# Kernel optimization log

Hardware: AMD Instinct MI355X
Metric: run time of the kernel (lower is better)

Reference implementation:

```python
import jax, jax.numpy as jnp
import numpy as np

N_NODES = 50000
N_EDGES = 500000
F_NODE, F_EDGE, D, H, L = 7, 8, 64, 128, 3


def setup_inputs() -> dict:
    key = jax.random.key(0)
    ks = jax.random.split(key, 24)
    g = lambda k, shp, fan: jax.random.normal(k, shp, dtype=jnp.float32) * (1.0 / np.sqrt(fan))
    inp = {
        "node_features": jax.random.normal(ks[0], (N_NODES, F_NODE), dtype=jnp.float32),
        "edge_attr": jax.random.normal(ks[1], (N_EDGES, F_EDGE), dtype=jnp.float32),
        "embed_W": g(ks[2], (F_NODE, D), F_NODE),
        "embed_b": jnp.zeros((D,), jnp.float32),
        "msg_W1": g(ks[3], (L, 2 * D + F_EDGE, H), 2 * D + F_EDGE),
        "msg_b1": jnp.zeros((L, H), jnp.float32),
        "msg_W2": g(ks[4], (L, H, H), H),
        "msg_b2": jnp.zeros((L, H), jnp.float32),
        "upd_W": g(ks[5], (L, D + H, D), D + H),
        "upd_b": jnp.zeros((L, D), jnp.float32),
        "ln_g": jnp.ones((L, D), jnp.float32),
        "ln_b": jnp.zeros((L, D), jnp.float32),
        "pred_W1": g(ks[6], (2 * D + F_EDGE, H), 2 * D + F_EDGE),
        "pred_b1": jnp.zeros((H,), jnp.float32),
        "pred_W2": g(ks[7], (H, H // 2), H),
        "pred_b2": jnp.zeros((H // 2,), jnp.float32),
        "pred_W3": g(ks[8], (H // 2, 1), H // 2),
        "pred_b3": jnp.zeros((1,), jnp.float32),
        "edge_index": jax.random.randint(ks[9], (2, N_EDGES), 0, N_NODES, dtype=jnp.int32),
    }
    return inp


def _layer_norm(x, g, b, eps=1e-5):
    mu = jnp.mean(x, axis=-1, keepdims=True)
    var = jnp.mean((x - mu) ** 2, axis=-1, keepdims=True)
    return (x - mu) * jax.lax.rsqrt(var + eps) * g + b


def reference(node_features, edge_attr, embed_W, embed_b, msg_W1, msg_b1, msg_W2, msg_b2,
              upd_W, upd_b, ln_g, ln_b, pred_W1, pred_b1, pred_W2, pred_b2, pred_W3, pred_b3,
              edge_index):
    src, dst = edge_index[0], edge_index[1]
    n_nodes = node_features.shape[0]
    # node embedding (dropout = identity in eval)
    x = jax.nn.relu(node_features @ embed_W + embed_b)
    ones_e = jnp.ones((edge_attr.shape[0],), dtype=x.dtype)
    counts = jax.ops.segment_sum(ones_e, dst, num_segments=n_nodes)[:, None]  # [N,1]
    for l in range(L):
        # gather + concat -> message MLP over edges
        edge_in = jnp.concatenate([x[src], x[dst], edge_attr], axis=1)  # [E, 2D+Fe]
        h = jax.nn.relu(edge_in @ msg_W1[l] + msg_b1[l])
        messages = h @ msg_W2[l] + msg_b2[l]  # [E, H]
        # scatter-add aggregation + mean normalize
        agg = jax.ops.segment_sum(messages, dst, num_segments=n_nodes)
        agg = agg / (counts + 1e-6)
        # update MLP with residual
        upd_in = jnp.concatenate([x, agg], axis=1)  # [N, D+H]
        x = x + jax.nn.relu(upd_in @ upd_W[l] + upd_b[l])
        x = _layer_norm(x, ln_g[l], ln_b[l])
    # edge predictor
    edge_in = jnp.concatenate([x[src], x[dst], edge_attr], axis=1)
    h = jax.nn.relu(edge_in @ pred_W1 + pred_b1)
    h = jax.nn.relu(h @ pred_W2 + pred_b2)
    pred = jnp.tanh(h @ pred_W3 + pred_b3)[:, 0]  # [E]
    return pred
```

## Files before the change

kernel.cpp:

```cpp
#include <hip/hip_runtime.h>

#define NN 50000
#define NE 500000
#define NBLK ((NN + 1023) / 1024)

typedef __attribute__((ext_vector_type(8))) short bf8_t;
typedef __attribute__((ext_vector_type(4))) float f4_t;
#define MFMA16(a, b, c) __builtin_amdgcn_mfma_f32_16x16x32_bf16(a, b, c, 0, 0, 0)

__device__ __forceinline__ short f2bf(float f) {
  unsigned u = __float_as_uint(f);
  u += 0x7fffu + ((u >> 16) & 1u);
  return (short)(u >> 16);
}
__device__ __forceinline__ float bf_lo(unsigned u) { return __uint_as_float(u << 16); }
__device__ __forceinline__ float bf_hi(unsigned u) { return __uint_as_float(u & 0xffff0000u); }
__device__ __forceinline__ float bf2f(short s) {
  return __uint_as_float(((unsigned)(unsigned short)s) << 16);
}

__global__ __launch_bounds__(256) void k_zero_i(int* __restrict__ p, int n)
{
  for (int i = blockIdx.x * 256 + threadIdx.x; i < n; i += gridDim.x * 256)
    p[i] = 0;
}

__global__ __launch_bounds__(256) void k_prep_w1(const float* __restrict__ W1,
                                                 short* __restrict__ w1f)
{
  int idx = blockIdx.x * 256 + threadIdx.x;
  if (idx >= 3 * 5 * 8 * 64 * 8) return;
  int l = idx / 20480;
  int rem = idx - l * 20480;
  int ks = rem / 4096;
  int nt = (rem >> 9) & 7;
  int lane = (rem >> 3) & 63;
  int j = rem & 7;
  int k = ks * 32 + (lane >> 4) * 8 + j;
  int n = nt * 16 + (lane & 15);
  float v = (k < 136) ? W1[(size_t)l * 136 * 128 + (size_t)k * 128 + n] : 0.f;
  w1f[idx] = f2bf(v);
}
__global__ __launch_bounds__(256) void k_prep_w2(const float* __restrict__ W2,
                                                 short* __restrict__ w2f)
{
  int idx = blockIdx.x * 256 + threadIdx.x;
  if (idx >= 3 * 4 * 8 * 64 * 8) return;
  int l = idx / 16384;
  int rem = idx - l * 16384;
  int ks = rem / 4096;
  int nt = (rem >> 9) & 7;
  int lane = (rem >> 3) & 63;
  int j = rem & 7;
  int k = ks * 32 + (lane >> 4) * 8 + j;
  int n = nt * 16 + (lane & 15);
  w2f[idx] = f2bf(W2[(size_t)l * 128 * 128 + (size_t)k * 128 + n]);
}
__global__ __launch_bounds__(256) void k_prep_wu(const float* __restrict__ Wu,
                                                 short* __restrict__ wuf)
{
  int idx = blockIdx.x * 256 + threadIdx.x;
  if (idx >= 3 * 6 * 4 * 64 * 8) return;
  int l = idx / 12288;
  int rem = idx - l * 12288;
  int ks = rem / 2048;
  int nt = (rem >> 9) & 3;
  int lane = (rem >> 3) & 63;
  int j = rem & 7;
  int k = ks * 32 + (lane >> 4) * 8 + j;
  int n = nt * 16 + (lane & 15);
  wuf[idx] = f2bf(Wu[(size_t)l * 192 * 64 + (size_t)k * 64 + n]);
}
__global__ __launch_bounds__(256) void k_prep_pw1(const float* __restrict__ W1,
                                                  short* __restrict__ wf)
{
  int idx = blockIdx.x * 256 + threadIdx.x;
  if (idx >= 5 * 8 * 64 * 8) return;
  int ks = idx / 4096;
  int nt = (idx >> 9) & 7;
  int lane = (idx >> 3) & 63;
  int j = idx & 7;
  int k = ks * 32 + (lane >> 4) * 8 + j;
  int n = nt * 16 + (lane & 15);
  float v = (k < 136) ? W1[(size_t)k * 128 + n] : 0.f;
  wf[idx] = f2bf(v);
}
__global__ __launch_bounds__(256) void k_prep_pw2(const float* __restrict__ W2,
                                                  short* __restrict__ wf)
{
  int idx = blockIdx.x * 256 + threadIdx.x;
  if (idx >= 4 * 4 * 64 * 8) return;
  int ks = idx / 2048;
  int nt = (idx >> 9) & 3;
  int lane = (idx >> 3) & 63;
  int j = idx & 7;
  int k = ks * 32 + (lane >> 4) * 8 + j;
  int n = nt * 16 + (lane & 15);
  wf[idx] = f2bf(W2[(size_t)k * 64 + n]);
}
__global__ __launch_bounds__(256) void k_prep_ea(const float* __restrict__ ea,
                                                 short* __restrict__ eab)
{
  int i = blockIdx.x * 256 + threadIdx.x;
  if (i >= NE * 2) return;
  float4 v = *(const float4*)&ea[(size_t)i * 4];
  short4 o;
  o.x = f2bf(v.x); o.y = f2bf(v.y); o.z = f2bf(v.z); o.w = f2bf(v.w);
  *(short4*)&eab[(size_t)i * 4] = o;
}

__global__ __launch_bounds__(256) void k_embed(
    const float* __restrict__ nf, const float* __restrict__ We,
    const float* __restrict__ be, float* __restrict__ x, short* __restrict__ xb)
{
  int idx = blockIdx.x * 256 + threadIdx.x;
  int n = idx >> 4, g = idx & 15;
  if (n >= NN) return;
  int j0 = g * 4;
  float4 b4 = *(const float4*)&be[j0];
  float a0 = b4.x, a1 = b4.y, a2 = b4.z, a3 = b4.w;
  #pragma unroll
  for (int k = 0; k < 7; ++k) {
    float v = nf[n * 7 + k];
    float4 w = *(const float4*)&We[k * 64 + j0];
    a0 += v * w.x; a1 += v * w.y; a2 += v * w.z; a3 += v * w.w;
  }
  a0 = fmaxf(a0, 0.f); a1 = fmaxf(a1, 0.f); a2 = fmaxf(a2, 0.f); a3 = fmaxf(a3, 0.f);
  *(float4*)&x[(size_t)n * 64 + j0] = make_float4(a0, a1, a2, a3);
  short4 o; o.x = f2bf(a0); o.y = f2bf(a1); o.z = f2bf(a2); o.w = f2bf(a3);
  *(short4*)&xb[(size_t)n * 64 + j0] = o;
}

__global__ __launch_bounds__(256) void k_hist(const int* __restrict__ dst, int* __restrict__ cnt)
{
  int e = blockIdx.x * 256 + threadIdx.x;
  if (e < NE) atomicAdd(&cnt[dst[e]], 1);
}

__global__ __launch_bounds__(1024) void k_scan1(const int* __restrict__ cnt,
                                                int* __restrict__ loc, int* __restrict__ bsum)
{
  __shared__ int ws[16];
  const int b = blockIdx.x, t = threadIdx.x;
  const int i = b * 1024 + t;
  const int ln = t & 63, wv = t >> 6;
  int v = (i < NN) ? cnt[i] : 0;
  int s = v;
  #pragma unroll
  for (int off = 1; off < 64; off <<= 1) {
    int u = __shfl_up(s, off, 64);
    if (ln >= off) s += u;
  }
  if (ln == 63) ws[wv] = s;
  __syncthreads();
  if (wv == 0) {
    int wsum = (ln < 16) ? ws[ln] : 0;
    #pragma unroll
    for (int off = 1; off < 16; off <<= 1) {
      int u = __shfl_up(wsum, off, 64);
      if (ln >= off) wsum += u;
    }
    if (ln < 16) ws[ln] = wsum;
  }
  __syncthreads();
  int woff = (wv > 0) ? ws[wv - 1] : 0;
  int incl = s + woff;
  if (i < NN) loc[i] = incl - v;
  if (t == 1023) bsum[b] = incl;
}
__global__ __launch_bounds__(64) void k_scan2(const int* __restrict__ bsum,
                                              int* __restrict__ boff)
{
  const int ln = threadIdx.x;
  int v = (ln < NBLK) ? bsum[ln] : 0;
  int s = v;
  #pragma unroll
  for (int off = 1; off < 64; off <<= 1) {
    int u = __shfl_up(s, off, 64);
    if (ln >= off) s += u;
  }
  if (ln < NBLK) boff[ln] = s - v;
}
__global__ __launch_bounds__(256) void k_scan3(const int* __restrict__ loc,
                                               const int* __restrict__ boff,
                                               int* __restrict__ ptr,
                                               int* __restrict__ cur)
{
  int i = blockIdx.x * 256 + threadIdx.x;
  if (i < NN) {
    int v = loc[i] + boff[i >> 10];
    ptr[i] = v;
    cur[i] = v;
  }
}

__global__ __launch_bounds__(256) void k_fill(
    const int* __restrict__ src, const int* __restrict__ dst,
    const short* __restrict__ eab, int* __restrict__ cur,
    int* __restrict__ srcc, short* __restrict__ eac)
{
  int e = blockIdx.x * 256 + threadIdx.x;
  if (e < 128) srcc[NE + e] = 0;
  if (e < NE) {
    int d = dst[e];
    int s = atomicAdd(&cur[d], 1);
    srcc[s] = src[e];
    *(bf8_t*)(eac + (size_t)s * 8) = *(const bf8_t*)(eab + (size_t)e * 8);
  }
}

__global__ __launch_bounds__(256, 4) void k_y1(
    const short* __restrict__ xb, const short* __restrict__ w1f_l,
    const float* __restrict__ b1,
    short* __restrict__ y1s, short* __restrict__ y1d)
{
  const int t = threadIdx.x;
  const int wv = t >> 6, l = t & 63;
  const int m16 = l & 15, g = l >> 4;
  const int nb = blockIdx.x * 64 + wv * 16;
  if (nb >= NN) return;
  int row = nb + m16; if (row >= NN) row = NN - 1;
  const short* xr = xb + (size_t)row * 64;
  bf8_t a0 = *(const bf8_t*)(xr + g * 8);
  bf8_t a1 = *(const bf8_t*)(xr + 32 + g * 8);
  const short* wl = w1f_l + l * 8;

  f4_t accS[8], accD[8];
  #pragma unroll
  for (int nt = 0; nt < 8; ++nt) {
    float bv = b1[nt * 16 + m16];
    accS[nt] = (f4_t){0.f, 0.f, 0.f, 0.f};
    accD[nt] = (f4_t){bv, bv, bv, bv};
  }
  #pragma unroll
  for (int nt = 0; nt < 8; ++nt) {
    bf8_t b0 = *(const bf8_t*)(wl + (0 * 8 + nt) * 512);
    bf8_t b1f = *(const bf8_t*)(wl + (1 * 8 + nt) * 512);
    bf8_t b2f = *(const bf8_t*)(wl + (2 * 8 + nt) * 512);
    bf8_t b3f = *(const bf8_t*)(wl + (3 * 8 + nt) * 512);
    accS[nt] = MFMA16(a0, b0, accS[nt]);
    accS[nt] = MFMA16(a1, b1f, accS[nt]);
    accD[nt] = MFMA16(a0, b2f, accD[nt]);
    accD[nt] = MFMA16(a1, b3f, accD[nt]);
  }
  #pragma unroll
  for (int nt = 0; nt < 8; ++nt) {
    #pragma unroll
    for (int r = 0; r < 4; ++r) {
      int n = nb + g * 4 + r;
      if (n < NN) {
        y1s[(size_t)n * 128 + nt * 16 + m16] = f2bf(accS[nt][r]);
        y1d[(size_t)n * 128 + nt * 16 + m16] = f2bf(accD[nt][r]);
      }
    }
  }
}

__global__ __launch_bounds__(256, 4) void k_msg_n(
    const short* __restrict__ y1s, const short* __restrict__ y1d,
    const short* __restrict__ eac, const int* __restrict__ srcc,
    const int* __restrict__ ptr, const int* __restrict__ cnt,
    const float* __restrict__ W1l,
    float* __restrict__ hagg)
{
  const int t = threadIdx.x;
  const int wv = t >> 6, ln = t & 63;
  const int n = blockIdx.x * 4 + wv;
  if (n >= NN) return;

  float we[8][2];
  #pragma unroll
  for (int f = 0; f < 8; ++f) {
    we[f][0] = W1l[(128 + f) * 128 + 2 * ln];
    we[f][1] = W1l[(128 + f) * 128 + 2 * ln + 1];
  }
  const int p0 = ptr[n];
  const int p1 = p0 + cnt[n];

  unsigned ydu = *(const unsigned*)(y1d + (size_t)n * 128 + 2 * ln);
  const float yd0 = bf_lo(ydu), yd1 = bf_hi(ydu);

  float s0 = 0.f, s1 = 0.f;
  for (int e = p0; e < p1; ++e) {
    int s = srcc[e];
    unsigned ysu = *(const unsigned*)(y1s + (size_t)s * 128 + 2 * ln);
    bf8_t eav = *(const bf8_t*)(eac + (size_t)e * 8);
    float z0 = 0.f, z1 = 0.f;
    #pragma unroll
    for (int f = 0; f < 8; ++f) {
      float ef = bf2f(eav[f]);
      z0 += ef * we[f][0];
      z1 += ef * we[f][1];
    }
    s0 += fmaxf(bf_lo(ysu) + yd0 + z0, 0.f);
    s1 += fmaxf(bf_hi(ysu) + yd1 + z1, 0.f);
  }
  *(float2*)(hagg + (size_t)n * 128 + 2 * ln) = make_float2(s0, s1);
}

__global__ __launch_bounds__(256, 4) void k_node(
    float* __restrict__ x, short* __restrict__ xb,
    const float* __restrict__ hagg, const int* __restrict__ cnt,
    const short* __restrict__ w2f_l, const float* __restrict__ b2,
    const short* __restrict__ wuf_l, const float* __restrict__ bu,
    const float* __restrict__ lng, const float* __restrict__ lnb)
{
  __shared__ short sH[4 * 16 * 136];
  const int t = threadIdx.x;
  const int wv = t >> 6, l = t & 63;
  const int m16 = l & 15, g = l >> 4;
  const int nb = blockIdx.x * 64 + wv * 16;
  if (nb >= NN) return;
  int row = nb + m16; if (row >= NN) row = NN - 1;

  const float* hr = hagg + (size_t)row * 128;
  bf8_t a2[4];
  #pragma unroll
  for (int ks = 0; ks < 4; ++ks) {
    float4 q0 = *(const float4*)(hr + ks * 32 + g * 8);
    float4 q1 = *(const float4*)(hr + ks * 32 + g * 8 + 4);
    bf8_t av = {f2bf(q0.x), f2bf(q0.y), f2bf(q0.z), f2bf(q0.w),
                f2bf(q1.x), f2bf(q1.y), f2bf(q1.z), f2bf(q1.w)};
    a2[ks] = av;
  }
  float dg[4], iv[4];
  #pragma unroll
  for (int r = 0; r < 4; ++r) {
    int n = nb + g * 4 + r;
    int c = (n < NN) ? cnt[n] : 0;
    dg[r] = (float)c;
    iv[r] = 1.f / ((float)c + 1e-6f);
  }

  const short* w2l = w2f_l + l * 8;
  f4_t aacc[8];
  #pragma unroll
  for (int nt = 0; nt < 8; ++nt) {
    float bv = b2[nt * 16 + m16];
    aacc[nt] = (f4_t){dg[0] * bv, dg[1] * bv, dg[2] * bv, dg[3] * bv};
  }
  #pragma unroll
  for (int ks = 0; ks < 4; ++ks) {
    #pragma unroll
    for (int nt = 0; nt < 8; ++nt) {
      bf8_t bf = *(const bf8_t*)(w2l + (ks * 8 + nt) * 512);
      aacc[nt] = MFMA16(a2[ks], bf, aacc[nt]);
    }
  }

  short* sh = sH + wv * (16 * 136);
  #pragma unroll
  for (int nt = 0; nt < 8; ++nt) {
    #pragma unroll
    for (int r = 0; r < 4; ++r) {
      sh[(g * 4 + r) * 136 + nt * 16 + m16] = f2bf(aacc[nt][r] * iv[r]);
    }
  }

  const short* xr = xb + (size_t)row * 64;
  bf8_t a0 = *(const bf8_t*)(xr + g * 8);
  bf8_t a1 = *(const bf8_t*)(xr + 32 + g * 8);
  const short* wul = wuf_l + l * 8;
  f4_t acc[4];
  #pragma unroll
  for (int nt = 0; nt < 4; ++nt) {
    float bv = bu[nt * 16 + m16];
    acc[nt] = (f4_t){bv, bv, bv, bv};
  }
  #pragma unroll
  for (int nt = 0; nt < 4; ++nt) {
    acc[nt] = MFMA16(a0, *(const bf8_t*)(wul + (0 * 4 + nt) * 512), acc[nt]);
    acc[nt] = MFMA16(a1, *(const bf8_t*)(wul + (1 * 4 + nt) * 512), acc[nt]);
  }
  #pragma unroll
  for (int ks = 0; ks < 4; ++ks) {
    bf8_t af = *(const bf8_t*)(sh + m16 * 136 + ks * 32 + g * 8);
    #pragma unroll
    for (int nt = 0; nt < 4; ++nt) {
      acc[nt] = MFMA16(af, *(const bf8_t*)(wul + ((2 + ks) * 4 + nt) * 512), acc[nt]);
    }
  }

  float ov[4][4];
  #pragma unroll
  for (int nt = 0; nt < 4; ++nt) {
    #pragma unroll
    for (int r = 0; r < 4; ++r) {
      int n = nb + g * 4 + r;
      float xv = (n < NN) ? x[(size_t)n * 64 + nt * 16 + m16] : 0.f;
      ov[nt][r] = xv + fmaxf(acc[nt][r], 0.f);
    }
  }
  #pragma unroll
  for (int r = 0; r < 4; ++r) {
    float s1 = ov[0][r] + ov[1][r] + ov[2][r] + ov[3][r];
    float s2 = ov[0][r] * ov[0][r] + ov[1][r] * ov[1][r] +
               ov[2][r] * ov[2][r] + ov[3][r] * ov[3][r];
    #pragma unroll
    for (int off = 1; off < 16; off <<= 1) {
      s1 += __shfl_xor(s1, off, 64);
      s2 += __shfl_xor(s2, off, 64);
    }
    float mu = s1 * 0.015625f;
    float var = s2 * 0.015625f - mu * mu;
    float rs = rsqrtf(var + 1e-5f);
    int n = nb + g * 4 + r;
    if (n < NN) {
      #pragma unroll
      for (int nt = 0; nt < 4; ++nt) {
        int col = nt * 16 + m16;
        float y = (ov[nt][r] - mu) * rs * lng[col] + lnb[col];
        x[(size_t)n * 64 + col] = y;
        xb[(size_t)n * 64 + col] = f2bf(y);
      }
    }
  }
}

__global__ __launch_bounds__(256, 4) void k_pred2(
    const short* __restrict__ py1s, const short* __restrict__ py1d,
    const short* __restrict__ eab,
    const int* __restrict__ src, const int* __restrict__ dst,
    const float* __restrict__ pW1,
    const short* __restrict__ pw2f, const float* __restrict__ b2,
    const float* __restrict__ W3, const float* __restrict__ b3,
    float* __restrict__ out)
{
  __shared__ short sH[4 * 16 * 136];
  const int t = threadIdx.x;
  const int wv = t >> 6, ln = t & 63;
  const int m16 = ln & 15, g = ln >> 4;
  const int p0 = blockIdx.x * 64 + wv * 16;
  if (p0 >= NE) return;

  float we[8][2];
  #pragma unroll
  for (int f = 0; f < 8; ++f) {
    we[f][0] = pW1[(128 + f) * 128 + 2 * ln];
    we[f][1] = pW1[(128 + f) * 128 + 2 * ln + 1];
  }
  const int li = ln & 15;
  int ei0 = p0 + li; if (ei0 >= NE) ei0 = NE - 1;
  int srcv = src[ei0];
  int dstv = dst[ei0];
  int ee = p0 + (ln >> 2); if (ee >= NE) ee = NE - 1;
  unsigned eaw = ((const unsigned*)eab)[(size_t)ee * 4 + (ln & 3)];

  unsigned ys[16], yd[16];
  #pragma unroll
  for (int i = 0; i < 16; ++i) {
    int s = __shfl(srcv, i, 64);
    int d = __shfl(dstv, i, 64);
    ys[i] = *(const unsigned*)(py1s + (size_t)s * 128 + 2 * ln);
    yd[i] = *(const unsigned*)(py1d + (size_t)d * 128 + 2 * ln);
  }

  short* sh = sH + wv * (16 * 136);
  #pragma unroll
  for (int i = 0; i < 16; ++i) {
    float z0 = 0.f, z1 = 0.f;
    #pragma unroll
    for (int w = 0; w < 4; ++w) {
      unsigned u = __shfl(eaw, 4 * i + w, 64);
      float e0 = bf_lo(u), e1 = bf_hi(u);
      z0 += e0 * we[2 * w][0] + e1 * we[2 * w + 1][0];
      z1 += e0 * we[2 * w][1] + e1 * we[2 * w + 1][1];
    }
    float h0 = fmaxf(bf_lo(ys[i]) + bf_lo(yd[i]) + z0, 0.f);
    float h1 = fmaxf(bf_hi(ys[i]) + bf_hi(yd[i]) + z1, 0.f);
    unsigned hv = (unsigned)(unsigned short)f2bf(h0) |
                  ((unsigned)(unsigned short)f2bf(h1) << 16);
    *(unsigned*)(sh + i * 136 + 2 * ln) = hv;
  }

  f4_t acc2[4];
  #pragma unroll
  for (int nt = 0; nt < 4; ++nt) {
    float bv = b2[nt * 16 + m16];
    acc2[nt] = (f4_t){bv, bv, bv, bv};
  }
  const short* w2l = pw2f + ln * 8;
  #pragma unroll
  for (int ks = 0; ks < 4; ++ks) {
    bf8_t af = *(const bf8_t*)(sh + m16 * 136 + ks * 32 + g * 8);
    #pragma unroll
    for (int nt = 0; nt < 4; ++nt) {
      bf8_t bf = *(const bf8_t*)(w2l + (ks * 4 + nt) * 512);
      acc2[nt] = MFMA16(af, bf, acc2[nt]);
    }
  }

  float w3v[4];
  #pragma unroll
  for (int nt = 0; nt < 4; ++nt) w3v[nt] = W3[nt * 16 + m16];
  const float b3v = b3[0];
  #pragma unroll
  for (int r = 0; r < 4; ++r) {
    float v = fmaxf(acc2[0][r], 0.f) * w3v[0] + fmaxf(acc2[1][r], 0.f) * w3v[1] +
              fmaxf(acc2[2][r], 0.f) * w3v[2] + fmaxf(acc2[3][r], 0.f) * w3v[3];
    #pragma unroll
    for (int off = 1; off < 16; off <<= 1) v += __shfl_xor(v, off, 64);
    int e = p0 + g * 4 + r;
    if (m16 == 0 && e < NE) out[e] = tanhf(v + b3v);
  }
}

extern "C" void kernel_launch(void* const* d_in, const int* in_sizes, int n_in,
                              void* d_out, int out_size, void* d_ws, size_t ws_size,
                              hipStream_t stream)
{
  (void)in_sizes; (void)n_in; (void)out_size; (void)ws_size;
  const float* nf  = (const float*)d_in[0];
  const float* ea  = (const float*)d_in[1];
  const float* eW  = (const float*)d_in[2];
  const float* eb  = (const float*)d_in[3];
  const float* mW1 = (const float*)d_in[4];
  const float* mb1 = (const float*)d_in[5];
  const float* mW2 = (const float*)d_in[6];
  const float* mb2 = (const float*)d_in[7];
  const float* uW  = (const float*)d_in[8];
  const float* ub  = (const float*)d_in[9];
  const float* lg  = (const float*)d_in[10];
  const float* lb  = (const float*)d_in[11];
  const float* pW1 = (const float*)d_in[12];
  const float* pb1 = (const float*)d_in[13];
  const float* pW2 = (const float*)d_in[14];
  const float* pb2 = (const float*)d_in[15];
  const float* pW3 = (const float*)d_in[16];
  const float* pb3 = (const float*)d_in[17];
  const int*   ei  = (const int*)d_in[18];
  const int* srcI = ei;
  const int* dstI = ei + NE;
  float* out = (float*)d_out;

  char* w = (char*)d_ws;
  float* x    = (float*)w;  w += (size_t)NN * 64 * 4;
  float* hagg = (float*)w;  w += (size_t)NN * 128 * 4;
  short* xb   = (short*)w;  w += (size_t)NN * 64 * 2;
  short* eab  = (short*)w;  w += (size_t)NE * 8 * 2;
  short* eac  = (short*)w;  w += (size_t)(NE + 128) * 8 * 2;
  short* y1s  = (short*)w;  w += (size_t)NN * 128 * 2;
  short* y1d  = (short*)w;  w += (size_t)NN * 128 * 2;
  short* w1f  = (short*)w;  w += (size_t)3 * 20480 * 2;
  short* w2f  = (short*)w;  w += (size_t)3 * 16384 * 2;
  short* wuf  = (short*)w;  w += (size_t)3 * 12288 * 2;
  short* pw1f = (short*)w;  w += (size_t)20480 * 2;
  short* pw2f = (short*)w;  w += (size_t)8192 * 2;
  int*   cnt  = (int*)w;    w += (size_t)NN * 4;
  int*   loc  = (int*)w;    w += (size_t)NN * 4;
  int*   ptr  = (int*)w;    w += (size_t)NN * 4;
  int*   cur  = (int*)w;    w += (size_t)NN * 4;
  int*   bsum = (int*)w;    w += (size_t)64 * 4;
  int*   boff = (int*)w;    w += (size_t)64 * 4;
  int*   srcc = (int*)w;    w += (size_t)(NE + 128) * 4;

  k_zero_i<<<64, 256, 0, stream>>>(cnt, NN);
  k_embed<<<(NN * 16 + 255) / 256, 256, 0, stream>>>(nf, eW, eb, x, xb);
  k_hist<<<(NE + 255) / 256, 256, 0, stream>>>(dstI, cnt);
  k_scan1<<<NBLK, 1024, 0, stream>>>(cnt, loc, bsum);
  k_scan2<<<1, 64, 0, stream>>>(bsum, boff);
  k_scan3<<<(NN + 255) / 256, 256, 0, stream>>>(loc, boff, ptr, cur);
  k_prep_ea<<<(NE * 2 + 255) / 256, 256, 0, stream>>>(ea, eab);
  k_fill<<<(NE + 255) / 256, 256, 0, stream>>>(srcI, dstI, eab, cur, srcc, eac);
  k_prep_w1<<<240, 256, 0, stream>>>(mW1, w1f);
  k_prep_w2<<<192, 256, 0, stream>>>(mW2, w2f);
  k_prep_wu<<<144, 256, 0, stream>>>(uW, wuf);
  k_prep_pw1<<<80, 256, 0, stream>>>(pW1, pw1f);
  k_prep_pw2<<<32, 256, 0, stream>>>(pW2, pw2f);

  const int ngrid = (NN + 63) / 64;
  const int egrid = (NE + 63) / 64;
  const int mgrid = (NN + 3) / 4;
  for (int l = 0; l < 3; ++l) {
    k_y1<<<ngrid, 256, 0, stream>>>(xb, w1f + (size_t)l * 20480,
        mb1 + (size_t)l * 128, y1s, y1d);
    k_msg_n<<<mgrid, 256, 0, stream>>>(y1s, y1d, eac, srcc, ptr, cnt,
        mW1 + (size_t)l * 136 * 128, hagg);
    k_node<<<ngrid, 256, 0, stream>>>(x, xb, hagg, cnt,
        w2f + (size_t)l * 16384, mb2 + (size_t)l * 128,
        wuf + (size_t)l * 12288, ub + (size_t)l * 64,
        lg + (size_t)l * 64, lb + (size_t)l * 64);
  }
  k_y1<<<ngrid, 256, 0, stream>>>(xb, pw1f, pb1, y1s, y1d);
  k_pred2<<<egrid, 256, 0, stream>>>(y1s, y1d, eab, srcI, dstI,
      pW1, pw2f, pb2, pW3, pb3, out);
}
```

Before: 537.8 us.

## Fuse embed and next-layer projection into node kernels, merge weight prep

Folds the embedding into the first y1 projection kernel and moves each later y1 projection into the end of k_node, reusing the layer-normed rows already staged in shared memory. Merges the five weight-prep kernels into one launch. Edge attributes are now kept in CSR order as fp32 rather than bf16, k_msg_n processes two edges per iteration, and its launch bound rises to 8 blocks. The aim is fewer launches and fewer re-reads of x, at the cost of more register pressure in k_node and double the edge-attribute bytes read in the message kernel.

```diff
diff --git a/kernel.cpp b/kernel.cpp
--- a/kernel.cpp
+++ b/kernel.cpp
@@ -15,9 +15,6 @@
 }
 __device__ __forceinline__ float bf_lo(unsigned u) { return __uint_as_float(u << 16); }
 __device__ __forceinline__ float bf_hi(unsigned u) { return __uint_as_float(u & 0xffff0000u); }
-__device__ __forceinline__ float bf2f(short s) {
-  return __uint_as_float(((unsigned)(unsigned short)s) << 16);
-}
 
 __global__ __launch_bounds__(256) void k_zero_i(int* __restrict__ p, int n)
 {
@@ -25,79 +22,69 @@
     p[i] = 0;
 }
 
-__global__ __launch_bounds__(256) void k_prep_w1(const float* __restrict__ W1,
-                                                 short* __restrict__ w1f)
+__global__ __launch_bounds__(256) void k_prep_all(
+    const float* __restrict__ mW1, const float* __restrict__ mW2,
+    const float* __restrict__ uW,
+    const float* __restrict__ pW1, const float* __restrict__ pW2,
+    short* __restrict__ w1f, short* __restrict__ w2f, short* __restrict__ wuf,
+    short* __restrict__ pw1f, short* __restrict__ pw2f)
 {
   int idx = blockIdx.x * 256 + threadIdx.x;
-  if (idx >= 3 * 5 * 8 * 64 * 8) return;
-  int l = idx / 20480;
-  int rem = idx - l * 20480;
-  int ks = rem / 4096;
-  int nt = (rem >> 9) & 7;
-  int lane = (rem >> 3) & 63;
-  int j = rem & 7;
-  int k = ks * 32 + (lane >> 4) * 8 + j;
-  int n = nt * 16 + (lane & 15);
-  float v = (k < 136) ? W1[(size_t)l * 136 * 128 + (size_t)k * 128 + n] : 0.f;
-  w1f[idx] = f2bf(v);
-}
-__global__ __launch_bounds__(256) void k_prep_w2(const float* __restrict__ W2,
-                                                 short* __restrict__ w2f)
-{
-  int idx = blockIdx.x * 256 + threadIdx.x;
-  if (idx >= 3 * 4 * 8 * 64 * 8) return;
-  int l = idx / 16384;
-  int rem = idx - l * 16384;
-  int ks = rem / 4096;
-  int nt = (rem >> 9) & 7;
-  int lane = (rem >> 3) & 63;
-  int j = rem & 7;
-  int k = ks * 32 + (lane >> 4) * 8 + j;
-  int n = nt * 16 + (lane & 15);
-  w2f[idx] = f2bf(W2[(size_t)l * 128 * 128 + (size_t)k * 128 + n]);
-}
-__global__ __launch_bounds__(256) void k_prep_wu(const float* __restrict__ Wu,
-                                                 short* __restrict__ wuf)
-{
-  int idx = blockIdx.x * 256 + threadIdx.x;
-  if (idx >= 3 * 6 * 4 * 64 * 8) return;
-  int l = idx / 12288;
-  int rem = idx - l * 12288;
-  int ks = rem / 2048;
-  int nt = (rem >> 9) & 3;
-  int lane = (rem >> 3) & 63;
-  int j = rem & 7;
-  int k = ks * 32 + (lane >> 4) * 8 + j;
-  int n = nt * 16 + (lane & 15);
-  wuf[idx] = f2bf(Wu[(size_t)l * 192 * 64 + (size_t)k * 64 + n]);
-}
-__global__ __launch_bounds__(256) void k_prep_pw1(const float* __restrict__ W1,
-                                                  short* __restrict__ wf)
-{
-  int idx = blockIdx.x * 256 + threadIdx.x;
-  if (idx >= 5 * 8 * 64 * 8) return;
-  int ks = idx / 4096;
-  int nt = (idx >> 9) & 7;
-  int lane = (idx >> 3) & 63;
-  int j = idx & 7;
-  int k = ks * 32 + (lane >> 4) * 8 + j;
-  int n = nt * 16 + (lane & 15);
-  float v = (k < 136) ? W1[(size_t)k * 128 + n] : 0.f;
-  wf[idx] = f2bf(v);
-}
-__global__ __launch_bounds__(256) void k_prep_pw2(const float* __restrict__ W2,
-                                                  short* __restrict__ wf)
-{
-  int idx = blockIdx.x * 256 + threadIdx.x;
-  if (idx >= 4 * 4 * 64 * 8) return;
-  int ks = idx / 2048;
-  int nt = (idx >> 9) & 3;
-  int lane = (idx >> 3) & 63;
-  int j = idx & 7;
-  int k = ks * 32 + (lane >> 4) * 8 + j;
-  int n = nt * 16 + (lane & 15);
-  wf[idx] = f2bf(W2[(size_t)k * 64 + n]);
-}
+  if (idx < 61440) {
+    int l = idx / 20480;
+    int rem = idx - l * 20480;
+    int ks = rem / 4096;
+    int nt = (rem >> 9) & 7;
+    int lane = (rem >> 3) & 63;
+    int j = rem & 7;
+    int k = ks * 32 + (lane >> 4) * 8 + j;
+    int n = nt * 16 + (lane & 15);
+    float v = (k < 136) ? mW1[(size_t)l * 136 * 128 + (size_t)k * 128 + n] : 0.f;
+    w1f[idx] = f2bf(v);
+  } else if (idx < 110592) {
+    int i2 = idx - 61440;
+    int l = i2 / 16384;
+    int rem = i2 - l * 16384;
+    int ks = rem / 4096;
+    int nt = (rem >> 9) & 7;
+    int lane = (rem >> 3) & 63;
+    int j = rem & 7;
+    int k = ks * 32 + (lane >> 4) * 8 + j;
+    int n = nt * 16 + (lane & 15);
+    w2f[i2] = f2bf(mW2[(size_t)l * 128 * 128 + (size_t)k * 128 + n]);
+  } else if (idx < 147456) {
+    int i3 = idx - 110592;
+    int l = i3 / 12288;
+    int rem = i3 - l * 12288;
+    int ks = rem / 2048;
+    int nt = (rem >> 9) & 3;
+    int lane = (rem >> 3) & 63;
+    int j = rem & 7;
+    int k = ks * 32 + (lane >> 4) * 8 + j;
+    int n = nt * 16 + (lane & 15);
+    wuf[i3] = f2bf(uW[(size_t)l * 192 * 64 + (size_t)k * 64 + n]);
+  } else if (idx < 167936) {
+    int i4 = idx - 147456;
+    int ks = i4 / 4096;
+    int nt = (i4 >> 9) & 7;
+    int lane = (i4 >> 3) & 63;
+    int j = i4 & 7;
+    int k = ks * 32 + (lane >> 4) * 8 + j;
+    int n = nt * 16 + (lane & 15);
+    float v = (k < 136) ? pW1[(size_t)k * 128 + n] : 0.f;
+    pw1f[i4] = f2bf(v);
+  } else if (idx < 176128) {
+    int i5 = idx - 167936;
+    int ks = i5 / 2048;
+    int nt = (i5 >> 9) & 3;
+    int lane = (i5 >> 3) & 63;
+    int j = i5 & 7;
+    int k = ks * 32 + (lane >> 4) * 8 + j;
+    int n = nt * 16 + (lane & 15);
+    pw2f[i5] = f2bf(pW2[(size_t)k * 64 + n]);
+  }
+}
+
 __global__ __launch_bounds__(256) void k_prep_ea(const float* __restrict__ ea,
                                                  short* __restrict__ eab)
 {
@@ -109,28 +96,6 @@
   *(short4*)&eab[(size_t)i * 4] = o;
 }
 
-__global__ __launch_bounds__(256) void k_embed(
-    const float* __restrict__ nf, const float* __restrict__ We,
-    const float* __restrict__ be, float* __restrict__ x, short* __restrict__ xb)
-{
-  int idx = blockIdx.x * 256 + threadIdx.x;
-  int n = idx >> 4, g = idx & 15;
-  if (n >= NN) return;
-  int j0 = g * 4;
-  float4 b4 = *(const float4*)&be[j0];
-  float a0 = b4.x, a1 = b4.y, a2 = b4.z, a3 = b4.w;
-  #pragma unroll
-  for (int k = 0; k < 7; ++k) {
-    float v = nf[n * 7 + k];
-    float4 w = *(const float4*)&We[k * 64 + j0];
-    a0 += v * w.x; a1 += v * w.y; a2 += v * w.z; a3 += v * w.w;
-  }
-  a0 = fmaxf(a0, 0.f); a1 = fmaxf(a1, 0.f); a2 = fmaxf(a2, 0.f); a3 = fmaxf(a3, 0.f);
-  *(float4*)&x[(size_t)n * 64 + j0] = make_float4(a0, a1, a2, a3);
-  short4 o; o.x = f2bf(a0); o.y = f2bf(a1); o.z = f2bf(a2); o.w = f2bf(a3);
-  *(short4*)&xb[(size_t)n * 64 + j0] = o;
-}
-
 __global__ __launch_bounds__(256) void k_hist(const int* __restrict__ dst, int* __restrict__ cnt)
 {
   int e = blockIdx.x * 256 + threadIdx.x;
@@ -196,8 +161,8 @@
 
 __global__ __launch_bounds__(256) void k_fill(
     const int* __restrict__ src, const int* __restrict__ dst,
-    const short* __restrict__ eab, int* __restrict__ cur,
-    int* __restrict__ srcc, short* __restrict__ eac)
+    const float* __restrict__ ea, int* __restrict__ cur,
+    int* __restrict__ srcc, float* __restrict__ eacf)
 {
   int e = blockIdx.x * 256 + threadIdx.x;
   if (e < 128) srcc[NE + e] = 0;
@@ -205,13 +170,18 @@
     int d = dst[e];
     int s = atomicAdd(&cur[d], 1);
     srcc[s] = src[e];
-    *(bf8_t*)(eac + (size_t)s * 8) = *(const bf8_t*)(eab + (size_t)e * 8);
-  }
-}
-
-__global__ __launch_bounds__(256, 4) void k_y1(
-    const short* __restrict__ xb, const short* __restrict__ w1f_l,
-    const float* __restrict__ b1,
+    float4 q0 = *(const float4*)(ea + (size_t)e * 8);
+    float4 q1 = *(const float4*)(ea + (size_t)e * 8 + 4);
+    *(float4*)(eacf + (size_t)s * 8) = q0;
+    *(float4*)(eacf + (size_t)s * 8 + 4) = q1;
+  }
+}
+
+__global__ __launch_bounds__(256, 4) void k_embed_y1(
+    const float* __restrict__ nf, const float* __restrict__ We,
+    const float* __restrict__ be,
+    const short* __restrict__ w1f0, const float* __restrict__ b10,
+    float* __restrict__ x, short* __restrict__ xb,
     short* __restrict__ y1s, short* __restrict__ y1d)
 {
   const int t = threadIdx.x;
@@ -219,16 +189,43 @@
   const int m16 = l & 15, g = l >> 4;
   const int nb = blockIdx.x * 64 + wv * 16;
   if (nb >= NN) return;
-  int row = nb + m16; if (row >= NN) row = NN - 1;
-  const short* xr = xb + (size_t)row * 64;
-  bf8_t a0 = *(const bf8_t*)(xr + g * 8);
-  bf8_t a1 = *(const bf8_t*)(xr + 32 + g * 8);
-  const short* wl = w1f_l + l * 8;
-
+  int row = nb + m16;
+  const bool valid = row < NN;
+  if (!valid) row = NN - 1;
+
+  float nfv[7];
+  #pragma unroll
+  for (int k = 0; k < 7; ++k) nfv[k] = nf[row * 7 + k];
+  float va[8], vb[8];
+  #pragma unroll
+  for (int j = 0; j < 8; ++j) {
+    int cA = g * 8 + j, cB = 32 + g * 8 + j;
+    float sa = be[cA], sb = be[cB];
+    #pragma unroll
+    for (int k = 0; k < 7; ++k) {
+      sa += nfv[k] * We[k * 64 + cA];
+      sb += nfv[k] * We[k * 64 + cB];
+    }
+    va[j] = fmaxf(sa, 0.f);
+    vb[j] = fmaxf(sb, 0.f);
+  }
+  bf8_t a0, a1;
+  #pragma unroll
+  for (int j = 0; j < 8; ++j) { a0[j] = f2bf(va[j]); a1[j] = f2bf(vb[j]); }
+  if (valid) {
+    *(float4*)&x[(size_t)row * 64 + g * 8]          = make_float4(va[0], va[1], va[2], va[3]);
+    *(float4*)&x[(size_t)row * 64 + g * 8 + 4]      = make_float4(va[4], va[5], va[6], va[7]);
+    *(float4*)&x[(size_t)row * 64 + 32 + g * 8]     = make_float4(vb[0], vb[1], vb[2], vb[3]);
+    *(float4*)&x[(size_t)row * 64 + 32 + g * 8 + 4] = make_float4(vb[4], vb[5], vb[6], vb[7]);
+    *(bf8_t*)(xb + (size_t)row * 64 + g * 8) = a0;
+    *(bf8_t*)(xb + (size_t)row * 64 + 32 + g * 8) = a1;
+  }
+
+  const short* wl = w1f0 + l * 8;
   f4_t accS[8], accD[8];
   #pragma unroll
   for (int nt = 0; nt < 8; ++nt) {
-    float bv = b1[nt * 16 + m16];
+    float bv = b10[nt * 16 + m16];
     accS[nt] = (f4_t){0.f, 0.f, 0.f, 0.f};
     accD[nt] = (f4_t){bv, bv, bv, bv};
   }
@@ -256,9 +253,9 @@
   }
 }
 
-__global__ __launch_bounds__(256, 4) void k_msg_n(
+__global__ __launch_bounds__(256, 8) void k_msg_n(
     const short* __restrict__ y1s, const short* __restrict__ y1d,
-    const short* __restrict__ eac, const int* __restrict__ srcc,
+    const float* __restrict__ eacf, const int* __restrict__ srcc,
     const int* __restrict__ ptr, const int* __restrict__ cnt,
     const float* __restrict__ W1l,
     float* __restrict__ hagg)
@@ -281,19 +278,40 @@
   const float yd0 = bf_lo(ydu), yd1 = bf_hi(ydu);
 
   float s0 = 0.f, s1 = 0.f;
-  for (int e = p0; e < p1; ++e) {
-    int s = srcc[e];
-    unsigned ysu = *(const unsigned*)(y1s + (size_t)s * 128 + 2 * ln);
-    bf8_t eav = *(const bf8_t*)(eac + (size_t)e * 8);
-    float z0 = 0.f, z1 = 0.f;
-    #pragma unroll
-    for (int f = 0; f < 8; ++f) {
-      float ef = bf2f(eav[f]);
-      z0 += ef * we[f][0];
-      z1 += ef * we[f][1];
-    }
-    s0 += fmaxf(bf_lo(ysu) + yd0 + z0, 0.f);
-    s1 += fmaxf(bf_hi(ysu) + yd1 + z1, 0.f);
+  int e = p0;
+  for (; e + 2 <= p1; e += 2) {
+    int sA = srcc[e];
+    int sB = srcc[e + 1];
+    unsigned ysA = *(const unsigned*)(y1s + (size_t)sA * 128 + 2 * ln);
+    unsigned ysB = *(const unsigned*)(y1s + (size_t)sB * 128 + 2 * ln);
+    float4 qa0 = *(const float4*)(eacf + (size_t)e * 8);
+    float4 qa1 = *(const float4*)(eacf + (size_t)e * 8 + 4);
+    float4 qb0 = *(const float4*)(eacf + (size_t)(e + 1) * 8);
+    float4 qb1 = *(const float4*)(eacf + (size_t)(e + 1) * 8 + 4);
+    float za0 = qa0.x * we[0][0] + qa0.y * we[1][0] + qa0.z * we[2][0] + qa0.w * we[3][0]
+              + qa1.x * we[4][0] + qa1.y * we[5][0] + qa1.z * we[6][0] + qa1.w * we[7][0];
+    float za1 = qa0.x * we[0][1] + qa0.y * we[1][1] + qa0.z * we[2][1] + qa0.w * we[3][1]
+              + qa1.x * we[4][1] + qa1.y * we[5][1] + qa1.z * we[6][1] + qa1.w * we[7][1];
+    float zb0 = qb0.x * we[0][0] + qb0.y * we[1][0] + qb0.z * we[2][0] + qb0.w * we[3][0]
+              + qb1.x * we[4][0] + qb1.y * we[5][0] + qb1.z * we[6][0] + qb1.w * we[7][0];
+    float zb1 = qb0.x * we[0][1] + qb0.y * we[1][1] + qb0.z * we[2][1] + qb0.w * we[3][1]
+              + qb1.x * we[4][1] + qb1.y * we[5][1] + qb1.z * we[6][1] + qb1.w * we[7][1];
+    s0 += fmaxf(bf_lo(ysA) + yd0 + za0, 0.f);
+    s1 += fmaxf(bf_hi(ysA) + yd1 + za1, 0.f);
+    s0 += fmaxf(bf_lo(ysB) + yd0 + zb0, 0.f);
+    s1 += fmaxf(bf_hi(ysB) + yd1 + zb1, 0.f);
+  }
+  if (e < p1) {
+    int sA = srcc[e];
+    unsigned ysA = *(const unsigned*)(y1s + (size_t)sA * 128 + 2 * ln);
+    float4 qa0 = *(const float4*)(eacf + (size_t)e * 8);
+    float4 qa1 = *(const float4*)(eacf + (size_t)e * 8 + 4);
+    float za0 = qa0.x * we[0][0] + qa0.y * we[1][0] + qa0.z * we[2][0] + qa0.w * we[3][0]
+              + qa1.x * we[4][0] + qa1.y * we[5][0] + qa1.z * we[6][0] + qa1.w * we[7][0];
+    float za1 = qa0.x * we[0][1] + qa0.y * we[1][1] + qa0.z * we[2][1] + qa0.w * we[3][1]
+              + qa1.x * we[4][1] + qa1.y * we[5][1] + qa1.z * we[6][1] + qa1.w * we[7][1];
+    s0 += fmaxf(bf_lo(ysA) + yd0 + za0, 0.f);
+    s1 += fmaxf(bf_hi(ysA) + yd1 + za1, 0.f);
   }
   *(float2*)(hagg + (size_t)n * 128 + 2 * ln) = make_float2(s0, s1);
 }
@@ -303,7 +321,9 @@
     const float* __restrict__ hagg, const int* __restrict__ cnt,
     const short* __restrict__ w2f_l, const float* __restrict__ b2,
     const short* __restrict__ wuf_l, const float* __restrict__ bu,
-    const float* __restrict__ lng, const float* __restrict__ lnb)
+    const float* __restrict__ lng, const float* __restrict__ lnb,
+    const short* __restrict__ wfn, const float* __restrict__ b1n,
+    short* __restrict__ y1s, short* __restrict__ y1d)
 {
   __shared__ short sH[4 * 16 * 136];
   const int t = threadIdx.x;
@@ -405,13 +425,48 @@
     float var = s2 * 0.015625f - mu * mu;
     float rs = rsqrtf(var + 1e-5f);
     int n = nb + g * 4 + r;
-    if (n < NN) {
-      #pragma unroll
-      for (int nt = 0; nt < 4; ++nt) {
-        int col = nt * 16 + m16;
-        float y = (ov[nt][r] - mu) * rs * lng[col] + lnb[col];
+    #pragma unroll
+    for (int nt = 0; nt < 4; ++nt) {
+      int col = nt * 16 + m16;
+      float y = (ov[nt][r] - mu) * rs * lng[col] + lnb[col];
+      short yb = f2bf(y);
+      sh[(g * 4 + r) * 136 + col] = yb;
+      if (n < NN) {
         x[(size_t)n * 64 + col] = y;
-        xb[(size_t)n * 64 + col] = f2bf(y);
+        xb[(size_t)n * 64 + col] = yb;
+      }
+    }
+  }
+
+  bf8_t ya0 = *(const bf8_t*)(sh + m16 * 136 + g * 8);
+  bf8_t ya1 = *(const bf8_t*)(sh + m16 * 136 + 32 + g * 8);
+  const short* wl = wfn + l * 8;
+  f4_t accS[8], accD[8];
+  #pragma unroll
+  for (int nt = 0; nt < 8; ++nt) {
+    float bv = b1n[nt * 16 + m16];
+    accS[nt] = (f4_t){0.f, 0.f, 0.f, 0.f};
+    accD[nt] = (f4_t){bv, bv, bv, bv};
+  }
+  #pragma unroll
+  for (int nt = 0; nt < 8; ++nt) {
+    bf8_t b0 = *(const bf8_t*)(wl + (0 * 8 + nt) * 512);
+    bf8_t b1f = *(const bf8_t*)(wl + (1 * 8 + nt) * 512);
+    bf8_t b2f = *(const bf8_t*)(wl + (2 * 8 + nt) * 512);
+    bf8_t b3f = *(const bf8_t*)(wl + (3 * 8 + nt) * 512);
+    accS[nt] = MFMA16(ya0, b0, accS[nt]);
+    accS[nt] = MFMA16(ya1, b1f, accS[nt]);
+    accD[nt] = MFMA16(ya0, b2f, accD[nt]);
+    accD[nt] = MFMA16(ya1, b3f, accD[nt]);
+  }
+  #pragma unroll
+  for (int nt = 0; nt < 8; ++nt) {
+    #pragma unroll
+    for (int r = 0; r < 4; ++r) {
+      int n = nb + g * 4 + r;
+      if (n < NN) {
+        y1s[(size_t)n * 128 + nt * 16 + m16] = f2bf(accS[nt][r]);
+        y1d[(size_t)n * 128 + nt * 16 + m16] = f2bf(accD[nt][r]);
       }
     }
   }
@@ -538,7 +593,7 @@
   float* hagg = (float*)w;  w += (size_t)NN * 128 * 4;
   short* xb   = (short*)w;  w += (size_t)NN * 64 * 2;
   short* eab  = (short*)w;  w += (size_t)NE * 8 * 2;
-  short* eac  = (short*)w;  w += (size_t)(NE + 128) * 8 * 2;
+  float* eacf = (float*)w;  w += (size_t)NE * 8 * 4;
   short* y1s  = (short*)w;  w += (size_t)NN * 128 * 2;
   short* y1d  = (short*)w;  w += (size_t)NN * 128 * 2;
   short* w1f  = (short*)w;  w += (size_t)3 * 20480 * 2;
@@ -555,33 +610,32 @@
   int*   srcc = (int*)w;    w += (size_t)(NE + 128) * 4;
 
   k_zero_i<<<64, 256, 0, stream>>>(cnt, NN);
-  k_embed<<<(NN * 16 + 255) / 256, 256, 0, stream>>>(nf, eW, eb, x, xb);
   k_hist<<<(NE + 255) / 256, 256, 0, stream>>>(dstI, cnt);
   k_scan1<<<NBLK, 1024, 0, stream>>>(cnt, loc, bsum);
   k_scan2<<<1, 64, 0, stream>>>(bsum, boff);
   k_scan3<<<(NN + 255) / 256, 256, 0, stream>>>(loc, boff, ptr, cur);
+  k_fill<<<(NE + 255) / 256, 256, 0, stream>>>(srcI, dstI, ea, cur, srcc, eacf);
   k_prep_ea<<<(NE * 2 + 255) / 256, 256, 0, stream>>>(ea, eab);
-  k_fill<<<(NE + 255) / 256, 256, 0, stream>>>(srcI, dstI, eab, cur, srcc, eac);
-  k_prep_w1<<<240, 256, 0, stream>>>(mW1, w1f);
-  k_prep_w2<<<192, 256, 0, stream>>>(mW2, w2f);
-  k_prep_wu<<<144, 256, 0, stream>>>(uW, wuf);
-  k_prep_pw1<<<80, 256, 0, stream>>>(pW1, pw1f);
-  k_prep_pw2<<<32, 256, 0, stream>>>(pW2, pw2f);
+  k_prep_all<<<(176128 + 255) / 256, 256, 0, stream>>>(
+      mW1, mW2, uW, pW1, pW2, w1f, w2f, wuf, pw1f, pw2f);
 
   const int ngrid = (NN + 63) / 64;
   const int egrid = (NE + 63) / 64;
   const int mgrid = (NN + 3) / 4;
+
+  k_embed_y1<<<ngrid, 256, 0, stream>>>(nf, eW, eb, w1f, mb1, x, xb, y1s, y1d);
+
   for (int l = 0; l < 3; ++l) {
-    k_y1<<<ngrid, 256, 0, stream>>>(xb, w1f + (size_t)l * 20480,
-        mb1 + (size_t)l * 128, y1s, y1d);
-    k_msg_n<<<mgrid, 256, 0, stream>>>(y1s, y1d, eac, srcc, ptr, cnt,
+    k_msg_n<<<mgrid, 256, 0, stream>>>(y1s, y1d, eacf, srcc, ptr, cnt,
         mW1 + (size_t)l * 136 * 128, hagg);
+    const short* wfn = (l < 2) ? (w1f + (size_t)(l + 1) * 20480) : pw1f;
+    const float* b1n = (l < 2) ? (mb1 + (size_t)(l + 1) * 128) : pb1;
     k_node<<<ngrid, 256, 0, stream>>>(x, xb, hagg, cnt,
         w2f + (size_t)l * 16384, mb2 + (size_t)l * 128,
         wuf + (size_t)l * 12288, ub + (size_t)l * 64,
-        lg + (size_t)l * 64, lb + (size_t)l * 64);
-  }
-  k_y1<<<ngrid, 256, 0, stream>>>(xb, pw1f, pb1, y1s, y1d);
+        lg + (size_t)l * 64, lb + (size_t)l * 64,
+        wfn, b1n, y1s, y1d);
+  }
   k_pred2<<<egrid, 256, 0, stream>>>(y1s, y1d, eab, srcI, dstI,
       pW1, pw2f, pb2, pW3, pb3, out);
 }
```

New measurement: 533.4 us. Within noise of the previous version (-0.8%).
